# Kernel tuning notes

Measured on AMD Instinct MI355X. Metric: run time of the kernel, lower is better.

Reference implementation:

```python
import jax, jax.numpy as jnp
import numpy as np
import math

K = 10      # number of propagation steps
BETA = 2.0  # log-weighting base
N_NODES = 100000
N_EDGES = 1000000
HIDDEN = 64


def setup_inputs() -> dict:
    key = jax.random.key(0)
    k1, k2, k3 = jax.random.split(key, 3)
    feat = jax.random.normal(k1, (N_NODES, HIDDEN), dtype=jnp.float32)
    src = jax.random.randint(k2, (N_EDGES,), 0, N_NODES, dtype=jnp.int64)
    dst = jax.random.randint(k3, (N_EDGES,), 0, N_NODES, dtype=jnp.int64)
    return {"feat": feat, "src": src, "dst": dst}


def reference(feat, src, dst):
    n = feat.shape[0]
    ones_e = jnp.ones(src.shape, dtype=feat.dtype)
    # out-degree of source nodes, in-degree of destination nodes
    out_deg = jax.ops.segment_sum(ones_e, src, num_segments=n)
    in_deg = jax.ops.segment_sum(ones_e, dst, num_segments=n)
    src_norm = jnp.maximum(out_deg, 1.0) ** -0.5  # [N]
    dst_norm = jnp.maximum(in_deg, 1.0) ** -0.5   # [N]

    # log-based combination weights over the K+1 snapshots
    logs = [math.log(BETA + i) for i in range(1, K + 2)]
    denom = sum(logs)
    w = [l / denom for l in logs]

    h = feat
    out = w[0] * feat
    for step in range(K):
        # gather-scale on source side, scatter-sum to destinations, scale on dst side
        m = (h * src_norm[:, None])[src]                      # [E, D]
        h = jax.ops.segment_sum(m, dst, num_segments=n)       # [N, D]
        h = h * dst_norm[:, None]
        out = out + w[step + 1] * h
    return out
```

## Files before the change

kernel.cpp:

```cpp
#include <hip/hip_runtime.h>
#include <hip/hip_bf16.h>
#include <math.h>

#define HIDDEN 64
#define K_STEPS 10
#define FULLN 102400
#define FULLW (FULLN / 4)
#define PADU 4

struct Wts { float v[K_STEPS + 1]; };

typedef float v2f __attribute__((ext_vector_type(2)));

__device__ __forceinline__ float bits2f(unsigned int u) {
    union { unsigned int i; float f; } c; c.i = u; return c.f;
}
__device__ __forceinline__ unsigned short f2bf(float f) {
    union { float f; unsigned int u; } c; c.f = f;
    unsigned int u = c.u;
    return (unsigned short)((u + 0x7FFF + ((u >> 16) & 1)) >> 16);
}
__device__ __forceinline__ void unpack_add(v2f acc[4], uint4 v) {
    v2f t;
    t.x = bits2f(v.x << 16); t.y = bits2f(v.x & 0xFFFF0000u); acc[0] += t;
    t.x = bits2f(v.y << 16); t.y = bits2f(v.y & 0xFFFF0000u); acc[1] += t;
    t.x = bits2f(v.z << 16); t.y = bits2f(v.z & 0xFFFF0000u); acc[2] += t;
    t.x = bits2f(v.w << 16); t.y = bits2f(v.w & 0xFFFF0000u); acc[3] += t;
}

__global__ void detect_kernel(const int* __restrict__ srcw,
                              const unsigned short* __restrict__ featw,
                              int* __restrict__ flags) {
    __shared__ int odd_nonzero;
    __shared__ int exp_in_range;
    if (threadIdx.x == 0) { odd_nonzero = 0; exp_in_range = 0; }
    __syncthreads();
    int w = srcw[2 * threadIdx.x + 1];
    if (w != 0) atomicAdd(&odd_nonzero, 1);
    unsigned short f = featw[2 * threadIdx.x];
    int ex = (f >> 7) & 0xFF;
    if (ex >= 90 && ex <= 135) atomicAdd(&exp_in_range, 1);
    __syncthreads();
    if (threadIdx.x == 0) {
        flags[0] = (odd_nonzero == 0) ? 1 : 0;
        flags[1] = (exp_in_range >= 240) ? 0 : 1;
    }
}

__global__ __launch_bounds__(1024) void hist_kernel(
        const void* __restrict__ src, const void* __restrict__ dst,
        const int* __restrict__ flags,
        unsigned* __restrict__ partials,
        unsigned char* __restrict__ rank,
        int E, int chunkE, int nchunks) {
    __shared__ unsigned bins[FULLW];
    int cx = blockIdx.x, az = blockIdx.y;
    for (int i = threadIdx.x; i < FULLW; i += 1024) bins[i] = 0;
    __syncthreads();
    const void* arr = az ? dst : src;
    int i64 = flags[0];
    int base = cx * chunkE;
    int lim = min(base + chunkE, E);
    for (int e = base + threadIdx.x; e < lim; e += 1024) {
        int v = i64 ? (int)((const long long*)arr)[e] : ((const int*)arr)[e];
        unsigned uv = (unsigned)v;
        int sh = (uv & 3) * 8;
        unsigned old = atomicAdd(&bins[uv >> 2], 1u << sh);
        if (az) rank[e] = (unsigned char)((old >> sh) & 0xFF);
    }
    __syncthreads();
    unsigned* out = partials + ((size_t)(az * nchunks + cx)) * FULLW;
    for (int i = threadIdx.x; i < FULLW; i += 1024) out[i] = bins[i];
}

__global__ void reduce_kernel(const unsigned* __restrict__ partials,
                              unsigned* __restrict__ chunk_pre,
                              int* __restrict__ out_deg, int* __restrict__ in_deg,
                              float* __restrict__ src_norm, float* __restrict__ dst_norm,
                              int N, int nchunks) {
    int t = blockIdx.x * blockDim.x + threadIdx.x;
    if (t >= 2 * FULLW) return;
    int a = t / FULLW;
    int lw = t % FULLW;
    const unsigned* p = partials + ((size_t)a * nchunks) * FULLW + lw;
    unsigned sum = 0;
    if (a == 1) {
        for (int c = 0; c < nchunks; ++c) {
            chunk_pre[(size_t)c * FULLW + lw] = sum;
            sum += p[(size_t)c * FULLW];
        }
    } else {
        for (int c = 0; c < nchunks; ++c) sum += p[(size_t)c * FULLW];
    }
    int nodeBase = lw * 4;
    int* deg = a ? in_deg : out_deg;
    float* nrm = a ? dst_norm : src_norm;
    #pragma unroll
    for (int k = 0; k < 4; ++k) {
        int n = nodeBase + k;
        if (n < N) {
            int d = (int)((sum >> (k * 8)) & 0xFF);
            deg[n] = d;
            nrm[n] = 1.0f / sqrtf(fmaxf((float)d, 1.0f));
        }
    }
}

__global__ void scanA_kernel(const int* __restrict__ deg, int* __restrict__ row_ptr,
                             int* __restrict__ block_sums, int N) {
    __shared__ int lds[256];
    int t = threadIdx.x;
    int base = blockIdx.x * 1024 + t * 4;
    int v0 = (base + 0 < N) ? ((deg[base + 0] + (PADU - 1)) & ~(PADU - 1)) : 0;
    int v1 = (base + 1 < N) ? ((deg[base + 1] + (PADU - 1)) & ~(PADU - 1)) : 0;
    int v2 = (base + 2 < N) ? ((deg[base + 2] + (PADU - 1)) & ~(PADU - 1)) : 0;
    int v3 = (base + 3 < N) ? ((deg[base + 3] + (PADU - 1)) & ~(PADU - 1)) : 0;
    int s = v0 + v1 + v2 + v3;
    lds[t] = s;
    __syncthreads();
    for (int off = 1; off < 256; off <<= 1) {
        int x = 0;
        if (t >= off) x = lds[t - off];
        __syncthreads();
        if (t >= off) lds[t] += x;
        __syncthreads();
    }
    int excl = lds[t] - s;
    if (t == 255) block_sums[blockIdx.x] = lds[255];
    if (base + 0 < N) row_ptr[base + 0] = excl;
    if (base + 1 < N) row_ptr[base + 1] = excl + v0;
    if (base + 2 < N) row_ptr[base + 2] = excl + v0 + v1;
    if (base + 3 < N) row_ptr[base + 3] = excl + v0 + v1 + v2;
}

__global__ void scanB_kernel(int* __restrict__ bs, int nb) {
    __shared__ int lds[1024];
    int t = threadIdx.x;
    int v = (t < nb) ? bs[t] : 0;
    lds[t] = v;
    __syncthreads();
    for (int off = 1; off < 1024; off <<= 1) {
        int x = 0;
        if (t >= off) x = lds[t - off];
        __syncthreads();
        if (t >= off) lds[t] += x;
        __syncthreads();
    }
    if (t < nb) bs[t] = lds[t] - v;
    if (t == nb - 1) bs[1024] = lds[t];
}

__global__ void scanC_pad_kernel(const int* __restrict__ raw_row,
                                 const int* __restrict__ block_offs,
                                 const int* __restrict__ in_deg,
                                 int* __restrict__ row_fin,
                                 int* __restrict__ col, int N) {
    int i = blockIdx.x * blockDim.x + threadIdx.x;
    if (i >= N) return;
    int b0 = raw_row[i] + block_offs[i >> 10];
    int b1 = (i + 1 < N) ? (raw_row[i + 1] + block_offs[(i + 1) >> 10])
                         : block_offs[1024];
    row_fin[i] = b0;
    if (i == 0) row_fin[N] = block_offs[1024];
    int s = b0 + in_deg[i];
    for (int j = s; j < b1; ++j) col[j] = N;
}

__global__ __launch_bounds__(1024) void scatter_kernel(
        const void* __restrict__ src, const void* __restrict__ dst,
        const int* __restrict__ flags,
        const int* __restrict__ row_fin,
        const unsigned* __restrict__ chunk_pre,
        const unsigned char* __restrict__ rank,
        int* __restrict__ col, int E, int chunkE) {
    __shared__ unsigned pre[FULLW];
    int cx = blockIdx.x;
    const unsigned* gpre = chunk_pre + (size_t)cx * FULLW;
    for (int i = threadIdx.x; i < FULLW; i += 1024) pre[i] = gpre[i];
    __syncthreads();
    int i64 = flags[0];
    int base = cx * chunkE;
    int lim = min(base + chunkE, E);
    for (int e = base + threadIdx.x; e < lim; e += 1024) {
        int s, d;
        if (i64) { s = (int)((const long long*)src)[e]; d = (int)((const long long*)dst)[e]; }
        else     { s = ((const int*)src)[e];            d = ((const int*)dst)[e]; }
        unsigned prew = pre[(unsigned)d >> 2];
        int pr = (int)((prew >> ((d & 3) * 8)) & 0xFF);
        col[row_fin[d] + pr + (int)rank[e]] = s;
    }
}

__global__ void init_kernel(const void* __restrict__ feat_raw,
                            const int* __restrict__ flags,
                            const float* __restrict__ src_norm,
                            uint4* __restrict__ hs8, float4* __restrict__ out_acc4,
                            float w0, int nchunks, int writeAcc,
                            int snapN, int nsnap) {
    int i = blockIdx.x * blockDim.x + threadIdx.x;
    if (i >= nchunks) {
        int j = i - nchunks;
        int k = j >> 3, r = j & 7;
        if (k < nsnap) {
            uint4 z; z.x = 0u; z.y = 0u; z.z = 0u; z.w = 0u;
            hs8[(size_t)k * snapN + nchunks + r] = z;
        }
        return;
    }
    int n = i >> 3;
    int c = i & 7;
    float sn = src_norm[n];
    float f[8];
    if (flags[1]) {
        float4 a = ((const float4*)feat_raw)[i * 2];
        float4 b = ((const float4*)feat_raw)[i * 2 + 1];
        f[0] = a.x; f[1] = a.y; f[2] = a.z; f[3] = a.w;
        f[4] = b.x; f[5] = b.y; f[6] = b.z; f[7] = b.w;
    } else {
        uint4 u = ((const uint4*)feat_raw)[i];
        f[0] = bits2f(u.x << 16); f[1] = bits2f(u.x & 0xFFFF0000u);
        f[2] = bits2f(u.y << 16); f[3] = bits2f(u.y & 0xFFFF0000u);
        f[4] = bits2f(u.z << 16); f[5] = bits2f(u.z & 0xFFFF0000u);
        f[6] = bits2f(u.w << 16); f[7] = bits2f(u.w & 0xFFFF0000u);
    }
    uint4 h;
    h.x = (unsigned int)f2bf(f[0] * sn) | ((unsigned int)f2bf(f[1] * sn) << 16);
    h.y = (unsigned int)f2bf(f[2] * sn) | ((unsigned int)f2bf(f[3] * sn) << 16);
    h.z = (unsigned int)f2bf(f[4] * sn) | ((unsigned int)f2bf(f[5] * sn) << 16);
    h.w = (unsigned int)f2bf(f[6] * sn) | ((unsigned int)f2bf(f[7] * sn) << 16);
    hs8[i] = h;
    if (writeAcc) {
        float4 o0, o1;
        o0.x = w0 * f[0]; o0.y = w0 * f[1]; o0.z = w0 * f[2]; o0.w = w0 * f[3];
        o1.x = w0 * f[4]; o1.y = w0 * f[5]; o1.z = w0 * f[6]; o1.w = w0 * f[7];
        size_t ob = (size_t)n * 16 + c * 2;
        out_acc4[ob] = o0;
        out_acc4[ob + 1] = o1;
    }
}

__device__ __forceinline__ void gather_row(const uint4* __restrict__ hs8,
                                           const int* __restrict__ col,
                                           int beg, int end, int fo,
                                           v2f a0[4], v2f a1[4]) {
    int e = beg;
    int nq = (end - beg) >> 2;
    if (nq & 1) {
        int4 c = *(const int4*)(col + e);
        uint4 v0 = hs8[((unsigned)c.x << 3) | fo];
        uint4 v1 = hs8[((unsigned)c.y << 3) | fo];
        uint4 v2 = hs8[((unsigned)c.z << 3) | fo];
        uint4 v3 = hs8[((unsigned)c.w << 3) | fo];
        unpack_add(a0, v0);
        unpack_add(a1, v1);
        unpack_add(a0, v2);
        unpack_add(a1, v3);
        e += 4;
    }
    if (e < end) {
        int4 c0 = *(const int4*)(col + e);
        int4 c1 = *(const int4*)(col + e + 4);
        for (;;) {
            int4 d0 = c0, d1 = c1;
            int ne = e + 8;
            if (ne < end) {
                c0 = *(const int4*)(col + ne);
                c1 = *(const int4*)(col + ne + 4);
            }
            uint4 v0 = hs8[((unsigned)d0.x << 3) | fo];
            uint4 v1 = hs8[((unsigned)d0.y << 3) | fo];
            uint4 v2 = hs8[((unsigned)d0.z << 3) | fo];
            uint4 v3 = hs8[((unsigned)d0.w << 3) | fo];
            uint4 v4 = hs8[((unsigned)d1.x << 3) | fo];
            uint4 v5 = hs8[((unsigned)d1.y << 3) | fo];
            uint4 v6 = hs8[((unsigned)d1.z << 3) | fo];
            uint4 v7 = hs8[((unsigned)d1.w << 3) | fo];
            unpack_add(a0, v0);
            unpack_add(a1, v1);
            unpack_add(a0, v2);
            unpack_add(a1, v3);
            unpack_add(a0, v4);
            unpack_add(a1, v5);
            unpack_add(a0, v6);
            unpack_add(a1, v7);
            e = ne;
            if (e >= end) break;
        }
    }
}

__global__ __launch_bounds__(256) void step_snap(
        const uint4* __restrict__ hs8, const int* __restrict__ row_fin,
        const int* __restrict__ col, const float* __restrict__ src_norm,
        const float* __restrict__ dst_norm, uint4* __restrict__ hs_next8, int N) {
    int wid = (blockIdx.x * 256 + threadIdx.x) >> 6;
    int nw = (gridDim.x * 256) >> 6;
    int lane = threadIdx.x & 63;
    int grp = lane >> 3, fo = lane & 7;
    for (int nbase = wid * 8; nbase < N; nbase += nw * 8) {
        int node = nbase + grp;
        int beg = 0, end = 0;
        if (node < N) { beg = row_fin[node]; end = row_fin[node + 1]; }
        v2f a0[4] = {v2f{0.f,0.f}, v2f{0.f,0.f}, v2f{0.f,0.f}, v2f{0.f,0.f}};
        v2f a1[4] = {v2f{0.f,0.f}, v2f{0.f,0.f}, v2f{0.f,0.f}, v2f{0.f,0.f}};
        if (beg < end) gather_row(hs8, col, beg, end, fo, a0, a1);
        if (node < N) {
            float m = dst_norm[node] * src_norm[node];
            #pragma unroll
            for (int k = 0; k < 4; ++k) a0[k] += a1[k];
            uint4 hn;
            hn.x = (unsigned int)f2bf(a0[0].x * m) | ((unsigned int)f2bf(a0[0].y * m) << 16);
            hn.y = (unsigned int)f2bf(a0[1].x * m) | ((unsigned int)f2bf(a0[1].y * m) << 16);
            hn.z = (unsigned int)f2bf(a0[2].x * m) | ((unsigned int)f2bf(a0[2].y * m) << 16);
            hn.w = (unsigned int)f2bf(a0[3].x * m) | ((unsigned int)f2bf(a0[3].y * m) << 16);
            hs_next8[((unsigned)node << 3) | fo] = hn;
        }
    }
}

__global__ __launch_bounds__(256) void step_last(
        const uint4* __restrict__ hs8, const int* __restrict__ row_fin,
        const int* __restrict__ col, const float* __restrict__ dst_norm,
        const void* __restrict__ feat_raw, const int* __restrict__ flags,
        const int* __restrict__ out_deg, const uint4* __restrict__ hs_base,
        float4* __restrict__ out4, Wts wts, int snapN, int N) {
    int wid = (blockIdx.x * 256 + threadIdx.x) >> 6;
    int nw = (gridDim.x * 256) >> 6;
    int lane = threadIdx.x & 63;
    int grp = lane >> 3, fo = lane & 7;
    for (int nbase = wid * 8; nbase < N; nbase += nw * 8) {
        int node = nbase + grp;
        int beg = 0, end = 0;
        if (node < N) { beg = row_fin[node]; end = row_fin[node + 1]; }
        v2f a0[4] = {v2f{0.f,0.f}, v2f{0.f,0.f}, v2f{0.f,0.f}, v2f{0.f,0.f}};
        v2f a1[4] = {v2f{0.f,0.f}, v2f{0.f,0.f}, v2f{0.f,0.f}, v2f{0.f,0.f}};
        if (beg < end) gather_row(hs8, col, beg, end, fo, a0, a1);
        if (node < N) {
            float dn = dst_norm[node];
            #pragma unroll
            for (int k = 0; k < 4; ++k) a0[k] += a1[k];
            int i = (node << 3) | fo;
            float acc[8];
            if (flags[1]) {
                float4 a = ((const float4*)feat_raw)[i * 2];
                float4 b = ((const float4*)feat_raw)[i * 2 + 1];
                acc[0] = a.x; acc[1] = a.y; acc[2] = a.z; acc[3] = a.w;
                acc[4] = b.x; acc[5] = b.y; acc[6] = b.z; acc[7] = b.w;
            } else {
                uint4 u = ((const uint4*)feat_raw)[i];
                acc[0] = bits2f(u.x << 16); acc[1] = bits2f(u.x & 0xFFFF0000u);
                acc[2] = bits2f(u.y << 16); acc[3] = bits2f(u.y & 0xFFFF0000u);
                acc[4] = bits2f(u.z << 16); acc[5] = bits2f(u.z & 0xFFFF0000u);
                acc[6] = bits2f(u.w << 16); acc[7] = bits2f(u.w & 0xFFFF0000u);
            }
            float w0 = wts.v[0];
            #pragma unroll
            for (int j = 0; j < 8; ++j) acc[j] *= w0;
            float inv = sqrtf(fmaxf((float)out_deg[node], 1.0f));
            #pragma unroll
            for (int k = 1; k < K_STEPS; ++k) {
                uint4 u = hs_base[(size_t)k * snapN + i];
                float sc = wts.v[k] * inv;
                acc[0] += sc * bits2f(u.x << 16); acc[1] += sc * bits2f(u.x & 0xFFFF0000u);
                acc[2] += sc * bits2f(u.y << 16); acc[3] += sc * bits2f(u.y & 0xFFFF0000u);
                acc[4] += sc * bits2f(u.z << 16); acc[5] += sc * bits2f(u.z & 0xFFFF0000u);
                acc[6] += sc * bits2f(u.w << 16); acc[7] += sc * bits2f(u.w & 0xFFFF0000u);
            }
            float wK = wts.v[K_STEPS] * dn;
            acc[0] += wK * a0[0].x; acc[1] += wK * a0[0].y;
            acc[2] += wK * a0[1].x; acc[3] += wK * a0[1].y;
            acc[4] += wK * a0[2].x; acc[5] += wK * a0[2].y;
            acc[6] += wK * a0[3].x; acc[7] += wK * a0[3].y;
            float4 o0 = {acc[0], acc[1], acc[2], acc[3]};
            float4 o1 = {acc[4], acc[5], acc[6], acc[7]};
            out4[i * 2] = o0;
            out4[i * 2 + 1] = o1;
        }
    }
}

template <bool LAST>
__global__ __launch_bounds__(256) void step_acc(
        const uint4* __restrict__ hs8, const int* __restrict__ row_fin,
        const int* __restrict__ col, const float* __restrict__ src_norm,
        const float* __restrict__ dst_norm, uint4* __restrict__ hs_next8,
        float4* __restrict__ out_acc4, float4* __restrict__ out4, float w, int N) {
    int wid = (blockIdx.x * 256 + threadIdx.x) >> 6;
    int nw = (gridDim.x * 256) >> 6;
    int lane = threadIdx.x & 63;
    int grp = lane >> 3, fo = lane & 7;
    for (int nbase = wid * 8; nbase < N; nbase += nw * 8) {
        int node = nbase + grp;
        int beg = 0, end = 0;
        if (node < N) { beg = row_fin[node]; end = row_fin[node + 1]; }
        v2f a0[4] = {v2f{0.f,0.f}, v2f{0.f,0.f}, v2f{0.f,0.f}, v2f{0.f,0.f}};
        v2f a1[4] = {v2f{0.f,0.f}, v2f{0.f,0.f}, v2f{0.f,0.f}, v2f{0.f,0.f}};
        if (beg < end) gather_row(hs8, col, beg, end, fo, a0, a1);
        if (node < N) {
            #pragma unroll
            for (int k = 0; k < 4; ++k) a0[k] += a1[k];
            float dn = dst_norm[node];
            float h0 = a0[0].x * dn, h1 = a0[0].y * dn, h2 = a0[1].x * dn, h3 = a0[1].y * dn;
            float h4 = a0[2].x * dn, h5 = a0[2].y * dn, h6 = a0[3].x * dn, h7 = a0[3].y * dn;
            size_t ob = (size_t)node * 16 + fo * 2;
            float4 o0 = out_acc4[ob];
            float4 o1 = out_acc4[ob + 1];
            o0.x += w * h0; o0.y += w * h1; o0.z += w * h2; o0.w += w * h3;
            o1.x += w * h4; o1.y += w * h5; o1.z += w * h6; o1.w += w * h7;
            if (LAST) {
                out4[ob] = o0;
                out4[ob + 1] = o1;
            } else {
                out_acc4[ob] = o0;
                out_acc4[ob + 1] = o1;
                float sn = src_norm[node];
                uint4 hn;
                hn.x = (unsigned int)f2bf(h0 * sn) | ((unsigned int)f2bf(h1 * sn) << 16);
                hn.y = (unsigned int)f2bf(h2 * sn) | ((unsigned int)f2bf(h3 * sn) << 16);
                hn.z = (unsigned int)f2bf(h4 * sn) | ((unsigned int)f2bf(h5 * sn) << 16);
                hn.w = (unsigned int)f2bf(h6 * sn) | ((unsigned int)f2bf(h7 * sn) << 16);
                hs_next8[((unsigned)node << 3) | fo] = hn;
            }
        }
    }
}

extern "C" void kernel_launch(void* const* d_in, const int* in_sizes, int n_in,
                              void* d_out, int out_size, void* d_ws, size_t ws_size,
                              hipStream_t stream) {
    const void* feat_raw = d_in[0];
    const void* src_raw = d_in[1];
    const void* dst_raw = d_in[2];
    float4* out4 = (float4*)d_out;

    const int N = in_sizes[0] / HIDDEN;
    const int E = (in_sizes[1] > 1500000) ? in_sizes[1] / 2 : in_sizes[1];
    const int nchunks = N * 8;
    const int snapN = nchunks + 8;
    const int Ecap = E + (PADU - 1) * N + 16;

    auto align256 = [](size_t b) { return (b + 255) & ~(size_t)255; };
    size_t base_bytes = align256(2 * sizeof(int))
                      + align256((size_t)N * sizeof(int))
                      + align256((size_t)N * sizeof(int))
                      + align256((size_t)(N + 1) * sizeof(int))
                      + align256((size_t)(N + 1) * sizeof(int))
                      + align256(1025 * sizeof(int))
                      + align256((size_t)Ecap * sizeof(int))
                      + align256((size_t)N * sizeof(float))
                      + align256((size_t)N * sizeof(float))
                      + align256((size_t)E);
    auto hist_bytes = [&](int C) {
        return align256((size_t)2 * C * FULLW * sizeof(unsigned))
             + align256((size_t)C * FULLW * sizeof(unsigned));
    };
    size_t snap_bytes = align256((size_t)(K_STEPS + 1) * snapN * sizeof(uint4));
    size_t acc_bytes  = align256((size_t)2 * snapN * sizeof(uint4))
                      + align256((size_t)N * 16 * sizeof(float4));

    int chunkShift = 13;
    int CHc = (E + (1 << chunkShift) - 1) >> chunkShift;
    int snapMode;
    if (ws_size >= base_bytes + hist_bytes(CHc) + snap_bytes) {
        snapMode = 1;
    } else {
        chunkShift = 14;
        CHc = (E + (1 << chunkShift) - 1) >> chunkShift;
        if (ws_size >= base_bytes + hist_bytes(CHc) + snap_bytes) {
            snapMode = 1;
        } else if (ws_size >= base_bytes + hist_bytes(CHc) + acc_bytes) {
            snapMode = 0;
        } else {
            chunkShift = 15;
            CHc = (E + (1 << chunkShift) - 1) >> chunkShift;
            snapMode = 0;
        }
    }
    const int chunkE = 1 << chunkShift;

    char* p = (char*)d_ws;
    auto alloc = [&](size_t bytes) {
        char* r = p;
        p += (bytes + 255) & ~(size_t)255;
        return r;
    };
    int* flags = (int*)alloc(2 * sizeof(int));
    int* out_deg = (int*)alloc((size_t)N * sizeof(int));
    int* in_deg = (int*)alloc((size_t)N * sizeof(int));
    int* row_ptr = (int*)alloc((size_t)(N + 1) * sizeof(int));
    int* row_fin = (int*)alloc((size_t)(N + 1) * sizeof(int));
    int* block_sums = (int*)alloc(1025 * sizeof(int));
    int* col = (int*)alloc((size_t)Ecap * sizeof(int));
    float* src_norm = (float*)alloc((size_t)N * sizeof(float));
    float* dst_norm = (float*)alloc((size_t)N * sizeof(float));
    unsigned char* rank = (unsigned char*)alloc((size_t)E);
    unsigned* partials = (unsigned*)alloc((size_t)2 * CHc * FULLW * sizeof(unsigned));
    unsigned* chunk_pre = (unsigned*)alloc((size_t)CHc * FULLW * sizeof(unsigned));
    uint4* hs_region;
    float4* out_acc = nullptr;
    if (snapMode) {
        hs_region = (uint4*)alloc((size_t)(K_STEPS + 1) * snapN * sizeof(uint4));
    } else {
        hs_region = (uint4*)alloc((size_t)2 * snapN * sizeof(uint4));
        out_acc = (float4*)alloc((size_t)N * 16 * sizeof(float4));
    }

    double logs[K_STEPS + 1];
    double denom = 0.0;
    for (int i = 0; i < K_STEPS + 1; ++i) {
        logs[i] = log(2.0 + (double)(i + 1));
        denom += logs[i];
    }
    Wts wts;
    for (int i = 0; i < K_STEPS + 1; ++i) wts.v[i] = (float)(logs[i] / denom);

    detect_kernel<<<1, 256, 0, stream>>>((const int*)src_raw,
                                         (const unsigned short*)feat_raw, flags);
    hist_kernel<<<dim3(CHc, 2), 1024, 0, stream>>>(src_raw, dst_raw, flags,
                                                   partials, rank, E, chunkE, CHc);
    reduce_kernel<<<(2 * FULLW + 255) / 256, 256, 0, stream>>>(
        partials, chunk_pre, out_deg, in_deg, src_norm, dst_norm, N, CHc);

    int nb = (N + 1023) / 1024;
    scanA_kernel<<<nb, 256, 0, stream>>>(in_deg, row_ptr, block_sums, N);
    scanB_kernel<<<1, 1024, 0, stream>>>(block_sums, nb);
    scanC_pad_kernel<<<(N + 255) / 256, 256, 0, stream>>>(row_ptr, block_sums, in_deg,
                                                          row_fin, col, N);
    scatter_kernel<<<CHc, 1024, 0, stream>>>(src_raw, dst_raw, flags, row_fin,
                                             chunk_pre, rank, col, E, chunkE);

    const int nsnap = snapMode ? (K_STEPS + 1) : 2;
    init_kernel<<<(nchunks + nsnap * 8 + 255) / 256, 256, 0, stream>>>(
        feat_raw, flags, src_norm, hs_region, out_acc, wts.v[0], nchunks,
        snapMode ? 0 : 1, snapN, nsnap);

    const int work_blocks = (((N + 7) / 8) + 3) / 4;
    if (snapMode) {
        for (int step = 0; step < K_STEPS - 1; ++step) {
            const uint4* cur = hs_region + (size_t)step * snapN;
            uint4* nxt = hs_region + (size_t)(step + 1) * snapN;
            step_snap<<<work_blocks, 256, 0, stream>>>(cur, row_fin, col, src_norm,
                                                       dst_norm, nxt, N);
        }
        const uint4* last_in = hs_region + (size_t)(K_STEPS - 1) * snapN;
        step_last<<<work_blocks, 256, 0, stream>>>(
            last_in, row_fin, col, dst_norm, feat_raw, flags, out_deg,
            hs_region, out4, wts, snapN, N);
    } else {
        uint4* cur = hs_region;
        uint4* nxt = hs_region + snapN;
        for (int step = 0; step < K_STEPS; ++step) {
            if (step == K_STEPS - 1) {
                step_acc<true><<<work_blocks, 256, 0, stream>>>(
                    cur, row_fin, col, src_norm, dst_norm, nxt, out_acc, out4,
                    wts.v[step + 1], N);
            } else {
                step_acc<false><<<work_blocks, 256, 0, stream>>>(
                    cur, row_fin, col, src_norm, dst_norm, nxt, out_acc, out4,
                    wts.v[step + 1], N);
            }
            uint4* t = cur; cur = nxt; nxt = t;
        }
    }
}
```

Baseline: 367.4 us.

## Fuse reduce with scan, drop rank array, prefetch snapshots in final step

The reduce kernel now also performs the per-1024-node block scan of padded in-degrees, removing the separate scanA launch and its reread of in_deg. The per-edge rank byte array is no longer written during the histogram; the scatter instead takes slot offsets from atomics on its LDS copy of the chunk prefix, which removes an E-byte write and read. The final step issues its feature and snapshot loads before the gather so their latency can overlap with it. The edge order inside each CSR row now depends on atomic timing, so float summation order can differ from run to run.

```diff
diff --git a/kernel.cpp b/kernel.cpp
--- a/kernel.cpp
+++ b/kernel.cpp
@@ -6,6 +6,7 @@
 #define K_STEPS 10
 #define FULLN 102400
 #define FULLW (FULLN / 4)
+#define NBLK1K (FULLW / 256)
 #define PADU 4
 
 struct Wts { float v[K_STEPS + 1]; };
@@ -26,6 +27,12 @@
     t.x = bits2f(v.y << 16); t.y = bits2f(v.y & 0xFFFF0000u); acc[1] += t;
     t.x = bits2f(v.z << 16); t.y = bits2f(v.z & 0xFFFF0000u); acc[2] += t;
     t.x = bits2f(v.w << 16); t.y = bits2f(v.w & 0xFFFF0000u); acc[3] += t;
+}
+__device__ __forceinline__ void acc_snap(float acc[8], uint4 u, float sc) {
+    acc[0] += sc * bits2f(u.x << 16); acc[1] += sc * bits2f(u.x & 0xFFFF0000u);
+    acc[2] += sc * bits2f(u.y << 16); acc[3] += sc * bits2f(u.y & 0xFFFF0000u);
+    acc[4] += sc * bits2f(u.z << 16); acc[5] += sc * bits2f(u.z & 0xFFFF0000u);
+    acc[6] += sc * bits2f(u.w << 16); acc[7] += sc * bits2f(u.w & 0xFFFF0000u);
 }
 
 __global__ void detect_kernel(const int* __restrict__ srcw,
@@ -51,7 +58,6 @@
         const void* __restrict__ src, const void* __restrict__ dst,
         const int* __restrict__ flags,
         unsigned* __restrict__ partials,
-        unsigned char* __restrict__ rank,
         int E, int chunkE, int nchunks) {
     __shared__ unsigned bins[FULLW];
     int cx = blockIdx.x, az = blockIdx.y;
@@ -64,24 +70,24 @@
     for (int e = base + threadIdx.x; e < lim; e += 1024) {
         int v = i64 ? (int)((const long long*)arr)[e] : ((const int*)arr)[e];
         unsigned uv = (unsigned)v;
-        int sh = (uv & 3) * 8;
-        unsigned old = atomicAdd(&bins[uv >> 2], 1u << sh);
-        if (az) rank[e] = (unsigned char)((old >> sh) & 0xFF);
+        atomicAdd(&bins[uv >> 2], 1u << ((uv & 3) * 8));
     }
     __syncthreads();
     unsigned* out = partials + ((size_t)(az * nchunks + cx)) * FULLW;
     for (int i = threadIdx.x; i < FULLW; i += 1024) out[i] = bins[i];
 }
 
-__global__ void reduce_kernel(const unsigned* __restrict__ partials,
-                              unsigned* __restrict__ chunk_pre,
-                              int* __restrict__ out_deg, int* __restrict__ in_deg,
-                              float* __restrict__ src_norm, float* __restrict__ dst_norm,
-                              int N, int nchunks) {
-    int t = blockIdx.x * blockDim.x + threadIdx.x;
-    if (t >= 2 * FULLW) return;
-    int a = t / FULLW;
-    int lw = t % FULLW;
+__global__ __launch_bounds__(256) void reduce_scan_kernel(
+        const unsigned* __restrict__ partials,
+        unsigned* __restrict__ chunk_pre,
+        int* __restrict__ out_deg, int* __restrict__ in_deg,
+        float* __restrict__ src_norm, float* __restrict__ dst_norm,
+        int* __restrict__ row_ptr, int* __restrict__ block_sums,
+        int N, int nchunks) {
+    __shared__ int lds[256];
+    int a = blockIdx.y;
+    int t = threadIdx.x;
+    int lw = blockIdx.x * 256 + t;
     const unsigned* p = partials + ((size_t)a * nchunks) * FULLW + lw;
     unsigned sum = 0;
     if (a == 1) {
@@ -95,42 +101,38 @@
     int nodeBase = lw * 4;
     int* deg = a ? in_deg : out_deg;
     float* nrm = a ? dst_norm : src_norm;
+    int d[4];
     #pragma unroll
     for (int k = 0; k < 4; ++k) {
+        d[k] = (int)((sum >> (k * 8)) & 0xFF);
         int n = nodeBase + k;
         if (n < N) {
-            int d = (int)((sum >> (k * 8)) & 0xFF);
-            deg[n] = d;
-            nrm[n] = 1.0f / sqrtf(fmaxf((float)d, 1.0f));
-        }
-    }
-}
-
-__global__ void scanA_kernel(const int* __restrict__ deg, int* __restrict__ row_ptr,
-                             int* __restrict__ block_sums, int N) {
-    __shared__ int lds[256];
-    int t = threadIdx.x;
-    int base = blockIdx.x * 1024 + t * 4;
-    int v0 = (base + 0 < N) ? ((deg[base + 0] + (PADU - 1)) & ~(PADU - 1)) : 0;
-    int v1 = (base + 1 < N) ? ((deg[base + 1] + (PADU - 1)) & ~(PADU - 1)) : 0;
-    int v2 = (base + 2 < N) ? ((deg[base + 2] + (PADU - 1)) & ~(PADU - 1)) : 0;
-    int v3 = (base + 3 < N) ? ((deg[base + 3] + (PADU - 1)) & ~(PADU - 1)) : 0;
-    int s = v0 + v1 + v2 + v3;
-    lds[t] = s;
-    __syncthreads();
-    for (int off = 1; off < 256; off <<= 1) {
-        int x = 0;
-        if (t >= off) x = lds[t - off];
+            deg[n] = d[k];
+            nrm[n] = 1.0f / sqrtf(fmaxf((float)d[k], 1.0f));
+        }
+    }
+    if (a == 1) {
+        int v0 = (d[0] + (PADU - 1)) & ~(PADU - 1);
+        int v1 = (d[1] + (PADU - 1)) & ~(PADU - 1);
+        int v2 = (d[2] + (PADU - 1)) & ~(PADU - 1);
+        int v3 = (d[3] + (PADU - 1)) & ~(PADU - 1);
+        int s = v0 + v1 + v2 + v3;
+        lds[t] = s;
         __syncthreads();
-        if (t >= off) lds[t] += x;
-        __syncthreads();
-    }
-    int excl = lds[t] - s;
-    if (t == 255) block_sums[blockIdx.x] = lds[255];
-    if (base + 0 < N) row_ptr[base + 0] = excl;
-    if (base + 1 < N) row_ptr[base + 1] = excl + v0;
-    if (base + 2 < N) row_ptr[base + 2] = excl + v0 + v1;
-    if (base + 3 < N) row_ptr[base + 3] = excl + v0 + v1 + v2;
+        for (int off = 1; off < 256; off <<= 1) {
+            int x = 0;
+            if (t >= off) x = lds[t - off];
+            __syncthreads();
+            if (t >= off) lds[t] += x;
+            __syncthreads();
+        }
+        int excl = lds[t] - s;
+        if (t == 255) block_sums[blockIdx.x] = lds[255];
+        if (nodeBase + 0 < N) row_ptr[nodeBase + 0] = excl;
+        if (nodeBase + 1 < N) row_ptr[nodeBase + 1] = excl + v0;
+        if (nodeBase + 2 < N) row_ptr[nodeBase + 2] = excl + v0 + v1;
+        if (nodeBase + 3 < N) row_ptr[nodeBase + 3] = excl + v0 + v1 + v2;
+    }
 }
 
 __global__ void scanB_kernel(int* __restrict__ bs, int nb) {
@@ -171,7 +173,6 @@
         const int* __restrict__ flags,
         const int* __restrict__ row_fin,
         const unsigned* __restrict__ chunk_pre,
-        const unsigned char* __restrict__ rank,
         int* __restrict__ col, int E, int chunkE) {
     __shared__ unsigned pre[FULLW];
     int cx = blockIdx.x;
@@ -185,9 +186,9 @@
         int s, d;
         if (i64) { s = (int)((const long long*)src)[e]; d = (int)((const long long*)dst)[e]; }
         else     { s = ((const int*)src)[e];            d = ((const int*)dst)[e]; }
-        unsigned prew = pre[(unsigned)d >> 2];
-        int pr = (int)((prew >> ((d & 3) * 8)) & 0xFF);
-        col[row_fin[d] + pr + (int)rank[e]] = s;
+        int sh = (d & 3) * 8;
+        unsigned old = atomicAdd(&pre[(unsigned)d >> 2], 1u << sh);
+        col[row_fin[d] + (int)((old >> sh) & 0xFF)] = s;
     }
 }
 
@@ -330,43 +331,52 @@
     int grp = lane >> 3, fo = lane & 7;
     for (int nbase = wid * 8; nbase < N; nbase += nw * 8) {
         int node = nbase + grp;
+        bool valid = (node < N);
+        int i = valid ? ((node << 3) | fo) : 0;
+        float acc[8];
+        if (flags[1]) {
+            float4 a = ((const float4*)feat_raw)[i * 2];
+            float4 b = ((const float4*)feat_raw)[i * 2 + 1];
+            acc[0] = a.x; acc[1] = a.y; acc[2] = a.z; acc[3] = a.w;
+            acc[4] = b.x; acc[5] = b.y; acc[6] = b.z; acc[7] = b.w;
+        } else {
+            uint4 u = ((const uint4*)feat_raw)[i];
+            acc[0] = bits2f(u.x << 16); acc[1] = bits2f(u.x & 0xFFFF0000u);
+            acc[2] = bits2f(u.y << 16); acc[3] = bits2f(u.y & 0xFFFF0000u);
+            acc[4] = bits2f(u.z << 16); acc[5] = bits2f(u.z & 0xFFFF0000u);
+            acc[6] = bits2f(u.w << 16); acc[7] = bits2f(u.w & 0xFFFF0000u);
+        }
+        uint4 s1 = hs_base[(size_t)1 * snapN + i];
+        uint4 s2 = hs_base[(size_t)2 * snapN + i];
+        uint4 s3 = hs_base[(size_t)3 * snapN + i];
+        uint4 s4 = hs_base[(size_t)4 * snapN + i];
+        uint4 s5 = hs_base[(size_t)5 * snapN + i];
+        uint4 s6 = hs_base[(size_t)6 * snapN + i];
+        uint4 s7 = hs_base[(size_t)7 * snapN + i];
+        uint4 s8 = hs_base[(size_t)8 * snapN + i];
+        uint4 s9 = hs_base[(size_t)9 * snapN + i];
         int beg = 0, end = 0;
-        if (node < N) { beg = row_fin[node]; end = row_fin[node + 1]; }
+        if (valid) { beg = row_fin[node]; end = row_fin[node + 1]; }
         v2f a0[4] = {v2f{0.f,0.f}, v2f{0.f,0.f}, v2f{0.f,0.f}, v2f{0.f,0.f}};
         v2f a1[4] = {v2f{0.f,0.f}, v2f{0.f,0.f}, v2f{0.f,0.f}, v2f{0.f,0.f}};
         if (beg < end) gather_row(hs8, col, beg, end, fo, a0, a1);
-        if (node < N) {
-            float dn = dst_norm[node];
+        if (valid) {
             #pragma unroll
             for (int k = 0; k < 4; ++k) a0[k] += a1[k];
-            int i = (node << 3) | fo;
-            float acc[8];
-            if (flags[1]) {
-                float4 a = ((const float4*)feat_raw)[i * 2];
-                float4 b = ((const float4*)feat_raw)[i * 2 + 1];
-                acc[0] = a.x; acc[1] = a.y; acc[2] = a.z; acc[3] = a.w;
-                acc[4] = b.x; acc[5] = b.y; acc[6] = b.z; acc[7] = b.w;
-            } else {
-                uint4 u = ((const uint4*)feat_raw)[i];
-                acc[0] = bits2f(u.x << 16); acc[1] = bits2f(u.x & 0xFFFF0000u);
-                acc[2] = bits2f(u.y << 16); acc[3] = bits2f(u.y & 0xFFFF0000u);
-                acc[4] = bits2f(u.z << 16); acc[5] = bits2f(u.z & 0xFFFF0000u);
-                acc[6] = bits2f(u.w << 16); acc[7] = bits2f(u.w & 0xFFFF0000u);
-            }
             float w0 = wts.v[0];
             #pragma unroll
             for (int j = 0; j < 8; ++j) acc[j] *= w0;
             float inv = sqrtf(fmaxf((float)out_deg[node], 1.0f));
-            #pragma unroll
-            for (int k = 1; k < K_STEPS; ++k) {
-                uint4 u = hs_base[(size_t)k * snapN + i];
-                float sc = wts.v[k] * inv;
-                acc[0] += sc * bits2f(u.x << 16); acc[1] += sc * bits2f(u.x & 0xFFFF0000u);
-                acc[2] += sc * bits2f(u.y << 16); acc[3] += sc * bits2f(u.y & 0xFFFF0000u);
-                acc[4] += sc * bits2f(u.z << 16); acc[5] += sc * bits2f(u.z & 0xFFFF0000u);
-                acc[6] += sc * bits2f(u.w << 16); acc[7] += sc * bits2f(u.w & 0xFFFF0000u);
-            }
-            float wK = wts.v[K_STEPS] * dn;
+            acc_snap(acc, s1, wts.v[1] * inv);
+            acc_snap(acc, s2, wts.v[2] * inv);
+            acc_snap(acc, s3, wts.v[3] * inv);
+            acc_snap(acc, s4, wts.v[4] * inv);
+            acc_snap(acc, s5, wts.v[5] * inv);
+            acc_snap(acc, s6, wts.v[6] * inv);
+            acc_snap(acc, s7, wts.v[7] * inv);
+            acc_snap(acc, s8, wts.v[8] * inv);
+            acc_snap(acc, s9, wts.v[9] * inv);
+            float wK = wts.v[K_STEPS] * dst_norm[node];
             acc[0] += wK * a0[0].x; acc[1] += wK * a0[0].y;
             acc[2] += wK * a0[1].x; acc[3] += wK * a0[1].y;
             acc[4] += wK * a0[2].x; acc[5] += wK * a0[2].y;
@@ -448,8 +458,7 @@
                       + align256(1025 * sizeof(int))
                       + align256((size_t)Ecap * sizeof(int))
                       + align256((size_t)N * sizeof(float))
-                      + align256((size_t)N * sizeof(float))
-                      + align256((size_t)E);
+                      + align256((size_t)N * sizeof(float));
     auto hist_bytes = [&](int C) {
         return align256((size_t)2 * C * FULLW * sizeof(unsigned))
              + align256((size_t)C * FULLW * sizeof(unsigned));
@@ -493,7 +502,6 @@
     int* col = (int*)alloc((size_t)Ecap * sizeof(int));
     float* src_norm = (float*)alloc((size_t)N * sizeof(float));
     float* dst_norm = (float*)alloc((size_t)N * sizeof(float));
-    unsigned char* rank = (unsigned char*)alloc((size_t)E);
     unsigned* partials = (unsigned*)alloc((size_t)2 * CHc * FULLW * sizeof(unsigned));
     unsigned* chunk_pre = (unsigned*)alloc((size_t)CHc * FULLW * sizeof(unsigned));
     uint4* hs_region;
@@ -517,17 +525,15 @@
     detect_kernel<<<1, 256, 0, stream>>>((const int*)src_raw,
                                          (const unsigned short*)feat_raw, flags);
     hist_kernel<<<dim3(CHc, 2), 1024, 0, stream>>>(src_raw, dst_raw, flags,
-                                                   partials, rank, E, chunkE, CHc);
-    reduce_kernel<<<(2 * FULLW + 255) / 256, 256, 0, stream>>>(
-        partials, chunk_pre, out_deg, in_deg, src_norm, dst_norm, N, CHc);
-
-    int nb = (N + 1023) / 1024;
-    scanA_kernel<<<nb, 256, 0, stream>>>(in_deg, row_ptr, block_sums, N);
-    scanB_kernel<<<1, 1024, 0, stream>>>(block_sums, nb);
+                                                   partials, E, chunkE, CHc);
+    reduce_scan_kernel<<<dim3(NBLK1K, 2), 256, 0, stream>>>(
+        partials, chunk_pre, out_deg, in_deg, src_norm, dst_norm,
+        row_ptr, block_sums, N, CHc);
+    scanB_kernel<<<1, 1024, 0, stream>>>(block_sums, NBLK1K);
     scanC_pad_kernel<<<(N + 255) / 256, 256, 0, stream>>>(row_ptr, block_sums, in_deg,
                                                           row_fin, col, N);
     scatter_kernel<<<CHc, 1024, 0, stream>>>(src_raw, dst_raw, flags, row_fin,
-                                             chunk_pre, rank, col, E, chunkE);
+                                             chunk_pre, col, E, chunkE);
 
     const int nsnap = snapMode ? (K_STEPS + 1) : 2;
     init_kernel<<<(nchunks + nsnap * 8 + 255) / 256, 256, 0, stream>>>(
```

Result: no change. 363.0 us (-1.2%).
